# Kernel optimization log

Measured on AMD Instinct MI355X. Metric: run time of the kernel, lower is better.

## Reference

```python
import jax, jax.numpy as jnp
import numpy as np


def _ste_round(x):
    # straight-through rounding (Brevitas-style QAT)
    return x + jax.lax.stop_gradient(jnp.round(x) - x)


def _q_act_signed(x, s):
    # 4-bit signed activation fake-quant: int range [-8, 7]
    return jnp.clip(_ste_round(x / s), -8, 7) * s


def _q_relu(x, s):
    # QuantReLU: relu then 4-bit unsigned fake-quant, int range [0, 15]
    return jnp.clip(_ste_round(jax.nn.relu(x) / s), 0, 15) * s


def _q_weight(w):
    # 4-bit narrow-range per-tensor weight quant: scale = max|w|/7, range [-7, 7]
    s = jnp.max(jnp.abs(w)) / 7.0
    return jnp.clip(_ste_round(w / s), -7, 7) * s, s


def _q_bias(b, s):
    # Int32Bias: bias quantized at scale = act_scale * weight_scale (int32 range, no clamp)
    return _ste_round(b / s) * s


def _conv(x, w):
    return jax.lax.conv_general_dilated(
        x, w, (1, 1), 'VALID', dimension_numbers=('NCHW', 'OIHW', 'NCHW'))


def _maxpool_ceil(x, k=3, st=2):
    # MaxPool2d(3, 2, ceil_mode=True): pad right/bottom with -inf as needed
    def pad(n):
        out = -(-(n - k) // st) + 1
        return max(0, (out - 1) * st + k - n)
    ph, pw = pad(x.shape[2]), pad(x.shape[3])
    return jax.lax.reduce_window(
        x, -jnp.inf, jax.lax.max, (1, 1, k, k), (1, 1, st, st),
        [(0, 0), (0, 0), (0, ph), (0, pw)])


def reference(x, w1, b1, w2, b2, w3, b3, fw1, fb1, bw, bb, cw, cb,
              s_inp, s1, s2, s3, s4, s_bbox, s_conf):
    a = s_inp[0]
    x = _q_act_signed(x, a)                               # quant_inp
    # conv1 + relu1 + pool1
    wq, ws = _q_weight(w1)
    x = _conv(x, wq) + _q_bias(b1, a * ws)[None, :, None, None]
    a = s1[0]
    x = _maxpool_ceil(_q_relu(x, a))                      # [B,28,11,11]
    # conv2 + relu2 + pool2
    wq, ws = _q_weight(w2)
    x = _conv(x, wq) + _q_bias(b2, a * ws)[None, :, None, None]
    a = s2[0]
    x = _maxpool_ceil(_q_relu(x, a))                      # [B,48,4,4]
    # conv3 + relu3
    wq, ws = _q_weight(w3)
    x = _conv(x, wq) + _q_bias(b3, a * ws)[None, :, None, None]
    a = s3[0]
    x = _q_relu(x, a)                                     # [B,64,3,3]
    # QuantFlatten: transpose(3,2) then flatten -> [B, 576]
    x = jnp.transpose(x, (0, 1, 3, 2)).reshape(x.shape[0], -1)
    # fc1 + relu4
    wq, ws = _q_weight(fw1)
    x = x @ wq.T + _q_bias(fb1, a * ws)
    a = s4[0]
    x = _q_relu(x, a)                                     # [B,128]
    # heads
    wq, ws = _q_weight(bw)
    bbox = x @ wq.T + _q_bias(bb, a * ws)                 # [B,4]
    wq, ws = _q_weight(cw)
    conf = x @ wq.T + _q_bias(cb, a * ws)                 # [B,2]
    bbox = _q_act_signed(bbox, s_bbox[0])
    conf = _q_act_signed(conf, s_conf[0])
    return bbox, conf


def setup_inputs() -> dict:
    key = jax.random.key(0)
    ks = jax.random.split(key, 14)
    B = 4096
    f32 = jnp.float32
    return {
        'x': jax.random.normal(ks[0], (B, 3, 24, 24), f32),
        'w1': jax.random.normal(ks[1], (28, 3, 3, 3), f32) * 0.1,
        'b1': jax.random.normal(ks[2], (28,), f32) * 0.1,
        'w2': jax.random.normal(ks[3], (48, 28, 3, 3), f32) * 0.1,
        'b2': jax.random.normal(ks[4], (48,), f32) * 0.1,
        'w3': jax.random.normal(ks[5], (64, 48, 2, 2), f32) * 0.1,
        'b3': jax.random.normal(ks[6], (64,), f32) * 0.1,
        'fw1': jax.random.normal(ks[7], (128, 576), f32) * 0.05,
        'fb1': jax.random.normal(ks[8], (128,), f32) * 0.1,
        'bw': jax.random.normal(ks[9], (4, 128), f32) * 0.1,
        'bb': jax.random.normal(ks[10], (4,), f32) * 0.1,
        'cw': jax.random.normal(ks[11], (2, 128), f32) * 0.1,
        'cb': jax.random.normal(ks[12], (2,), f32) * 0.1,
        's_inp': jnp.ones((1,), f32),
        's1': jnp.ones((1,), f32),
        's2': jnp.ones((1,), f32),
        's3': jnp.ones((1,), f32),
        's4': jnp.ones((1,), f32),
        's_bbox': jnp.ones((1,), f32),
        's_conf': jnp.ones((1,), f32),
    }
```

## Files before the change

### kernel.cpp

```cpp
#include <hip/hip_runtime.h>
#include <hip/hip_bf16.h>
#include <math.h>

typedef __attribute__((ext_vector_type(8))) short bf16x8v;
typedef __attribute__((ext_vector_type(4))) float f32x4v;

__device__ __forceinline__ float loadT(const void* p, size_t i, int isbf) {
    if (isbf) return __bfloat162float(((const __hip_bfloat16*)p)[i]);
    return ((const float*)p)[i];
}
__device__ __forceinline__ float quantw(float v, float s) {
    return fminf(fmaxf(rintf(v / s), -7.f), 7.f) * s;
}
__device__ __forceinline__ float quantwc(float v, float s) {
    return fminf(fmaxf(rintf(v / s), -7.f), 7.f);
}
__device__ __forceinline__ float qbias(float v, float den) {
    return rintf(v / den) * den;
}
__device__ __forceinline__ float qrelu(float v, float s) {
    return fminf(fmaxf(rintf(fmaxf(v, 0.f) / s), 0.f), 15.f) * s;
}
__device__ __forceinline__ float qcode(float Cint, float bcode, float p, float snext) {
    float v = (Cint + bcode) * p;
    return fminf(fmaxf(rintf(fmaxf(v, 0.f) / snext), 0.f), 15.f);
}
__device__ __forceinline__ float bfbits(unsigned u) {
    return __uint_as_float(u << 16);
}

__global__ void k_beacon(float* out, float code) {
    if (threadIdx.x == 0 && blockIdx.x == 0) out[0] = code;
}

static constexpr int W1C  = 16;
static constexpr int B1C  = 772;
static constexpr int B2C  = 800;
static constexpr int B3C  = 848;
static constexpr int FB1C = 912;
static constexpr int BBC  = 1040;
static constexpr int CBC  = 1044;
static constexpr int FW1B = 1048;
static constexpr int W2B  = 37912;
static constexpr int W3B  = 44056;
static constexpr int BWC  = 50200;
static constexpr int CWC  = 50712;
static constexpr int PMAXF = 51000;

__device__ __constant__ int d_CHK[6]  = { 1, 4, 4, 24, 1, 1 };
__device__ __constant__ int d_POFF[7] = { 0, 1, 5, 9, 33, 34, 35 };

__global__ __launch_bounds__(256) void k_scale(
    const void* w1, const void* w2, const void* w3, const void* fw1,
    const void* bw, const void* cw,
    const void* s0p, const void* s1p, const void* s2p, const void* s3p,
    const void* s4p, const void* s5p, const void* s6p,
    float* __restrict__ ws)
{
    __shared__ float red[256];
    __shared__ float shisbf;
    const int tid = threadIdx.x, blk = blockIdx.x;
    if (tid < 64) {
        const unsigned short* hb = (const unsigned short*)w1;
        const float a = fabsf(bfbits((unsigned)hb[2 * tid]));
        const unsigned long long bz = __ballot(a == 0.f);
        const unsigned long long bs = __ballot(a > 1e-8f && a < 1e4f);
        if (tid == 0) {
            const int zeros = __popcll(bz), sane = __popcll(bs);
            shisbf = (zeros < 40 && sane >= 40) ? 1.f : 0.f;
        }
    }
    __syncthreads();
    const int isbf = shisbf > 0.5f;
    if (blk == 0) {
        if (tid == 7) ws[15] = shisbf;
        if (tid < 7) {
            const void* sp[7] = { s0p, s1p, s2p, s3p, s4p, s5p, s6p };
            const void* p = sp[tid];
            float v = *(const float*)p;
            float a = fabsf(v);
            if (!(a > 1e-6f && a < 1e6f)) {
                double d = *(const double*)p;
                double ad = fabs(d);
                if (ad > 1e-6 && ad < 1e6) v = (float)d;
                else v = bfbits((unsigned)(*(const unsigned short*)p));
            }
            ws[tid] = v;
        }
    }
    int j = 0;
    while (j < 5 && blk >= d_POFF[j + 1]) ++j;
    const int c = blk - d_POFF[j];
    const void* wp[6] = { w1, w2, w3, fw1, bw, cw };
    const int   wn[6] = { 756, 12096, 12288, 73728, 512, 256 };
    const int nw = wn[j];
    const int len = (nw + d_CHK[j] - 1) / d_CHK[j];
    const int i0 = c * len, i1 = min(i0 + len, nw);
    float m = 0.f;
    for (int i = i0 + tid; i < i1; i += 256)
        m = fmaxf(m, fabsf(loadT(wp[j], i, isbf)));
    red[tid] = m; __syncthreads();
    for (int o = 128; o > 0; o >>= 1) {
        if (tid < o) red[tid] = fmaxf(red[tid], red[tid + o]);
        __syncthreads();
    }
    if (tid == 0) ws[PMAXF + blk] = red[0];
}

__global__ __launch_bounds__(256) void k_quant(
    const void* w1, const void* b1, const void* w2, const void* b2,
    const void* w3, const void* b3, const void* fw1, const void* fb1,
    const void* bw, const void* bb, const void* cw, const void* cb,
    float* __restrict__ ws)
{
    const int tid = threadIdx.x, blk = blockIdx.x;
    const int isbf = ws[15] > 0.5f;
    auto getscale = [&](int j) {
        float m = 0.f;
        for (int t = d_POFF[j]; t < d_POFF[j + 1]; ++t)
            m = fmaxf(m, ws[PMAXF + t]);
        return m / 7.0f;
    };

    if (blk < 24) {
        const float s = getscale(3);
        const int i0 = blk * 3072, i1 = min(i0 + 3072, 73728);
        __hip_bfloat16* dst = (__hip_bfloat16*)(ws + FW1B);
        for (int i = i0 + tid; i < i1; i += 256) {
            const float q = quantwc(loadT(fw1, i, isbf), s);
            const int o = i / 576, f = i % 576;
            const int c = f / 9, fw_ = (f % 9) / 3, fh = f % 3;
            dst[(c * 9 + fh * 3 + fw_) * 128 + o] = __float2bfloat16(q);
        }
    } else if (blk < 28) {
        const float s = getscale(1);
        const int c = blk - 24;
        const int i0 = c * 3024, i1 = min(i0 + 3024, 12096);
        __hip_bfloat16* dst = (__hip_bfloat16*)(ws + W2B);
        for (int i = i0 + tid; i < i1; i += 256) {
            const float q = quantwc(loadT(w2, i, isbf), s);
            const int n = i / 252, k = i % 252;
            dst[n * 256 + k] = __float2bfloat16(q);
        }
        if (c == 0) {
            for (int i = tid; i < 192; i += 256) {
                const int n = i / 4, k = 252 + (i % 4);
                dst[n * 256 + k] = __float2bfloat16(0.f);
            }
        }
    } else if (blk < 32) {
        const float s = getscale(2);
        const int c = blk - 28;
        const int i0 = c * 3072, i1 = min(i0 + 3072, 12288);
        __hip_bfloat16* dst = (__hip_bfloat16*)(ws + W3B);
        for (int i = i0 + tid; i < i1; i += 256)
            dst[i] = __float2bfloat16(quantwc(loadT(w3, i, isbf), s));
    } else if (blk == 32) {
        const float s = getscale(0);
        for (int i = tid; i < 756; i += 256)
            ws[W1C + i] = quantwc(loadT(w1, i, isbf), s);
    } else {
        const float s0 = getscale(0), s1 = getscale(1), s2 = getscale(2);
        const float s3 = getscale(3), s4 = getscale(4), s5 = getscale(5);
        const float sa0 = ws[0], sa1 = ws[1], sa2 = ws[2], sa3 = ws[3], sa4 = ws[4];
        for (int i = tid; i < 512; i += 256) ws[BWC + i] = quantwc(loadT(bw, i, isbf), s4);
        for (int i = tid; i < 256; i += 256) ws[CWC + i] = quantwc(loadT(cw, i, isbf), s5);
        if (tid < 28)  ws[B1C + tid]  = rintf(loadT(b1, tid, isbf)  / (sa0 * s0));
        if (tid < 48)  ws[B2C + tid]  = rintf(loadT(b2, tid, isbf)  / (sa1 * s1));
        if (tid < 64)  ws[B3C + tid]  = rintf(loadT(b3, tid, isbf)  / (sa2 * s2));
        if (tid < 128) ws[FB1C + tid] = rintf(loadT(fb1, tid, isbf) / (sa3 * s3));
        if (tid < 4)   ws[BBC + tid]  = rintf(loadT(bb, tid, isbf)  / (sa4 * s4));
        if (tid < 2)   ws[CBC + tid]  = rintf(loadT(cb, tid, isbf)  / (sa4 * s5));
        if (tid == 0) {
            ws[8]  = sa0 * s0;
            ws[9]  = sa1 * s1;
            ws[10] = sa2 * s2;
            ws[11] = sa3 * s3;
            ws[12] = sa4 * s4;
            ws[13] = sa4 * s5;
        }
    }
}

__global__ __launch_bounds__(256, 4) void k_net(
    const void* __restrict__ x, const float* __restrict__ wsr,
    float* __restrict__ outp)
{
    __shared__ __align__(16) float U[9952];
    const int tid = threadIdx.x, b = blockIdx.x;
    const float sa0 = wsr[0], sa1 = wsr[1], sa2 = wsr[2], sa3 = wsr[3];
    const float sa4 = wsr[4], sab = wsr[5], sac = wsr[6];
    const float p1 = wsr[8], p2 = wsr[9], p3 = wsr[10], p4 = wsr[11];
    const float pB = wsr[12], pC = wsr[13];
    const int isbf = wsr[15] > 0.5f;
    constexpr int ACT2F = 0, ACT3F = 768, ACT1F = 1344;
    constexpr int XQF = 3040, W1F = 4840, B1F = 5596;
    constexpr int AF = 3040, BFP = 4960, C2IF = 5920, B2CF = 9889;
    constexpr int W3F = 3040, B3CF = 9184;
    constexpr int PF = 3040, A4F = 3296, PARTF = 3424;

    for (int i = tid; i < 1728; i += 256) {
        const float v = loadT(x, (size_t)b * 1728 + i, isbf);
        const int ci = i / 576, r = (i % 576) / 24, c = i % 24;
        U[XQF + ci * 600 + r * 25 + c] = fminf(fmaxf(rintf(v / sa0), -8.f), 7.f);
    }
    for (int i = tid; i < 756; i += 256) U[W1F + i] = wsr[W1C + i];
    if (tid < 28) U[B1F + tid] = wsr[B1C + tid];
    __syncthreads();

    {
        __hip_bfloat16* act1w = (__hip_bfloat16*)(U + ACT1F);
        for (int item = tid; item < 308; item += 256) {
            const int o = item / 11, ph = item % 11;
            const int r0 = 2 * ph;
            const bool row2ok = (r0 + 2) < 22;
            float wk[27];
            #pragma unroll
            for (int i = 0; i < 27; ++i) wk[i] = U[W1F + o * 27 + i];
            const float bc = U[B1F + o];
            float w5[45];
            #pragma unroll
            for (int ci = 0; ci < 3; ++ci)
                #pragma unroll
                for (int ir = 0; ir < 5; ++ir)
                    #pragma unroll
                    for (int j = 0; j < 2; ++j)
                        w5[ci * 15 + ir * 3 + j] =
                            (r0 + ir < 24) ? U[XQF + ci * 600 + (r0 + ir) * 25 + j] : 0.f;
            float accP = -1e30f, accC = -1e30f;
            for (int c = 0; c < 22; ++c) {
                #pragma unroll
                for (int ci = 0; ci < 3; ++ci)
                    #pragma unroll
                    for (int ir = 0; ir < 5; ++ir)
                        w5[ci * 15 + ir * 3 + 2] =
                            (r0 + ir < 24) ? U[XQF + ci * 600 + (r0 + ir) * 25 + (c + 2)] : 0.f;
                float a0 = 0.f, a1 = 0.f, a2 = 0.f;
                #pragma unroll
                for (int ci = 0; ci < 3; ++ci)
                    #pragma unroll
                    for (int kr = 0; kr < 3; ++kr)
                        #pragma unroll
                        for (int kc = 0; kc < 3; ++kc) {
                            const float w = wk[ci * 9 + kr * 3 + kc];
                            a0 = fmaf(w5[ci * 15 + (kr + 0) * 3 + kc], w, a0);
                            a1 = fmaf(w5[ci * 15 + (kr + 1) * 3 + kc], w, a1);
                            a2 = fmaf(w5[ci * 15 + (kr + 2) * 3 + kc], w, a2);
                        }
                float cm = fmaxf(a0, a1);
                cm = row2ok ? fmaxf(cm, a2) : cm;
                if ((c & 1) == 0) {
                    if (c >= 2)
                        act1w[o * 121 + ph * 11 + (c / 2 - 1)] =
                            __float2bfloat16(qcode(fmaxf(accP, cm), bc, p1, sa1));
                    accC = cm;
                } else {
                    accC = fmaxf(accC, cm);
                    accP = accC;
                }
                #pragma unroll
                for (int ci = 0; ci < 3; ++ci)
                    #pragma unroll
                    for (int ir = 0; ir < 5; ++ir) {
                        w5[ci * 15 + ir * 3 + 0] = w5[ci * 15 + ir * 3 + 1];
                        w5[ci * 15 + ir * 3 + 1] = w5[ci * 15 + ir * 3 + 2];
                    }
            }
            act1w[o * 121 + ph * 11 + 10] =
                __float2bfloat16(qcode(accP, bc, p1, sa1));
        }
    }
    __syncthreads();

    {
        const unsigned short* act1u = (const unsigned short*)(U + ACT1F);
        unsigned short* Au = (unsigned short*)(U + AF);
        unsigned short* Bu = (unsigned short*)(U + BFP);
        const unsigned short* w2u = (const unsigned short*)(wsr + W2B);
        if (tid < 48) U[B2CF + tid] = wsr[B2C + tid];
        const int kloc = tid & 31, g = tid >> 5;
        const int wv = tid >> 6, lane = tid & 63;
        f32x4v acc[5];
        #pragma unroll
        for (int j = 0; j < 5; ++j) { acc[j][0]=0.f; acc[j][1]=0.f; acc[j][2]=0.f; acc[j][3]=0.f; }
        for (int kk = 0; kk < 8; ++kk) {
            const int k = kk * 32 + kloc;
            const bool kok = (k < 252);
            const int ci = kok ? k / 9 : 0;
            const int kr = kok ? (k % 9) / 3 : 0, kc = kok ? k % 3 : 0;
            #pragma unroll
            for (int e = 0; e < 12; ++e) {
                const int s = g + 8 * e;
                unsigned short v = 0;
                if (kok && s < 81) {
                    const int r = s / 9, c = s % 9;
                    v = act1u[ci * 121 + (r + kr) * 11 + (c + kc)];
                }
                Au[s * 40 + kloc] = v;
            }
            #pragma unroll
            for (int e = 0; e < 6; ++e) {
                const int n = g + 8 * e;
                Bu[n * 40 + kloc] = w2u[n * 256 + k];
            }
            __syncthreads();
            #pragma unroll
            for (int j = 0; j < 5; ++j) {
                const int t = wv + 4 * j;
                if (t < 18) {
                    const int tm = t / 3, tn = t % 3;
                    bf16x8v af = *(const bf16x8v*)(Au + (tm * 16 + (lane & 15)) * 40 + (lane >> 4) * 8);
                    bf16x8v bfv = *(const bf16x8v*)(Bu + (tn * 16 + (lane & 15)) * 40 + (lane >> 4) * 8);
                    acc[j] = __builtin_amdgcn_mfma_f32_16x16x32_bf16(af, bfv, acc[j], 0, 0, 0);
                }
            }
            __syncthreads();
        }
        #pragma unroll
        for (int j = 0; j < 5; ++j) {
            const int t = wv + 4 * j;
            if (t < 18) {
                const int tm = t / 3, tn = t % 3;
                const int col = tn * 16 + (lane & 15);
                #pragma unroll
                for (int r = 0; r < 4; ++r) {
                    const int row = tm * 16 + (lane >> 4) * 4 + r;
                    if (row < 81) U[C2IF + row * 49 + col] = acc[j][r];
                }
            }
        }
        __syncthreads();
        for (int id = tid; id < 768; id += 256) {
            const int ch = id >> 4, pp = id & 15, ph = pp >> 2, pw = pp & 3;
            float mx = -1e30f;
            #pragma unroll
            for (int r = 0; r < 3; ++r)
                #pragma unroll
                for (int c = 0; c < 3; ++c)
                    mx = fmaxf(mx, U[C2IF + ((2 * ph + r) * 9 + (2 * pw + c)) * 49 + ch]);
            U[ACT2F + ch * 16 + pp] = qcode(mx, U[B2CF + ch], p2, sa2);
        }
    }
    __syncthreads();

    for (int i = tid; i < 6144; i += 256) U[W3F + i] = wsr[W3B + i];
    if (tid < 64) U[B3CF + tid] = wsr[B3C + tid];
    __syncthreads();
    if (tid < 192) {
        const int o = tid / 3, hq = tid % 3;
        const unsigned* w3u = (const unsigned*)(U + W3F);
        float a0 = 0.f, a1 = 0.f, a2 = 0.f;
        for (int ci = 0; ci < 48; ++ci) {
            const unsigned pa = w3u[o * 96 + ci * 2];
            const unsigned pb = w3u[o * 96 + ci * 2 + 1];
            const float w00 = bfbits(pa & 0xffffu), w01 = bfbits(pa >> 16);
            const float w10 = bfbits(pb & 0xffffu), w11 = bfbits(pb >> 16);
            const int xb = ACT2F + ci * 16;
            float r0[4], r1[4];
            #pragma unroll
            for (int c = 0; c < 4; ++c) {
                r0[c] = U[xb + hq * 4 + c];
                r1[c] = U[xb + (hq + 1) * 4 + c];
            }
            a0 = fmaf(r0[0], w00, a0); a0 = fmaf(r0[1], w01, a0);
            a0 = fmaf(r1[0], w10, a0); a0 = fmaf(r1[1], w11, a0);
            a1 = fmaf(r0[1], w00, a1); a1 = fmaf(r0[2], w01, a1);
            a1 = fmaf(r1[1], w10, a1); a1 = fmaf(r1[2], w11, a1);
            a2 = fmaf(r0[2], w00, a2); a2 = fmaf(r0[3], w01, a2);
            a2 = fmaf(r1[2], w10, a2); a2 = fmaf(r1[3], w11, a2);
        }
        const float bc = U[B3CF + o];
        U[ACT3F + o * 9 + hq * 3 + 0] = qcode(a0, bc, p3, sa3);
        U[ACT3F + o * 9 + hq * 3 + 1] = qcode(a1, bc, p3, sa3);
        U[ACT3F + o * 9 + hq * 3 + 2] = qcode(a2, bc, p3, sa3);
    }
    __syncthreads();

    {
        const int o = tid & 127, half = tid >> 7;
        const __hip_bfloat16* fwb = (const __hip_bfloat16*)(wsr + FW1B);
        float acc = 0.f;
        const int k0 = half * 288;
        for (int k = k0; k < k0 + 288; ++k)
            acc = fmaf(U[ACT3F + k], __bfloat162float(fwb[k * 128 + o]), acc);
        U[PF + tid] = acc;
    }
    __syncthreads();
    if (tid < 128) {
        const float C = U[PF + tid] + U[PF + 128 + tid];
        U[A4F + tid] = qcode(C, wsr[FB1C + tid], p4, sa4);
    }
    __syncthreads();

    if (tid < 96) {
        const int d = tid >> 4, gq = tid & 15;
        const float* hw = (d < 4) ? (wsr + BWC + d * 128) : (wsr + CWC + (d - 4) * 128);
        float p = 0.f;
        #pragma unroll
        for (int k = 0; k < 8; ++k)
            p = fmaf(U[A4F + gq * 8 + k], hw[gq * 8 + k], p);
        U[PARTF + d * 16 + gq] = p;
    }
    __syncthreads();
    if (tid < 6) {
        float C = (tid < 4) ? wsr[BBC + tid] : wsr[CBC + (tid - 4)];
        for (int g = 0; g < 16; ++g) C += U[PARTF + tid * 16 + g];
        if (tid < 4) {
            const float val = C * pB;
            outp[(size_t)b * 4 + tid] = fminf(fmaxf(rintf(val / sab), -8.f), 7.f) * sab;
        } else {
            const float val = C * pC;
            outp[16384 + (size_t)b * 2 + (tid - 4)] =
                fminf(fmaxf(rintf(val / sac), -8.f), 7.f) * sac;
        }
    }
}

__global__ __launch_bounds__(256) void k_net_fb(
    const void* __restrict__ x,
    const void* __restrict__ w1,  const void* __restrict__ b1,
    const void* __restrict__ w2,  const void* __restrict__ b2,
    const void* __restrict__ w3,  const void* __restrict__ b3,
    const void* __restrict__ fw1, const void* __restrict__ fb1,
    const void* __restrict__ bw,  const void* __restrict__ bb,
    const void* __restrict__ cw,  const void* __restrict__ cb,
    const void* __restrict__ s0p, const void* __restrict__ s1p,
    const void* __restrict__ s2p, const void* __restrict__ s3p,
    const void* __restrict__ s4p, const void* __restrict__ s5p,
    const void* __restrict__ s6p,
    float* __restrict__ outp)
{
    __shared__ float U[16000];
    __shared__ float swsh[8];
    __shared__ float sash[8];
    const int tid = threadIdx.x;
    const int b   = blockIdx.x;
    constexpr int RED = 0, XQ = 0, W1Q = 1728, B1Q = 2484, C1 = 2512;
    constexpr int ACT1 = 9288, WB = 0, C2 = 12676, ACT2 = 14620, ACT3 = 15388;
    constexpr int A4 = 0, PART = 128;

    if (tid == 0) {
        const unsigned short* hb = (const unsigned short*)w1;
        int zeros = 0, sane = 0;
        for (int i = 0; i < 64; ++i) {
            unsigned short u = hb[2 * i];
            float v = __uint_as_float(((unsigned int)u) << 16);
            float a = fabsf(v);
            if (a == 0.f) zeros++;
            else if (a > 1e-8f && a < 1e4f) sane++;
        }
        swsh[7] = (zeros < 40 && sane >= 40) ? 1.f : 0.f;
        const void* sp[7] = { s0p, s1p, s2p, s3p, s4p, s5p, s6p };
        for (int j = 0; j < 7; ++j) {
            float v = *(const float*)sp[j];
            float a = fabsf(v);
            if (!(a > 1e-6f && a < 1e6f)) {
                double d = *(const double*)sp[j];
                double ad = fabs(d);
                if (ad > 1e-6 && ad < 1e6) v = (float)d;
                else {
                    unsigned short u = *(const unsigned short*)sp[j];
                    v = __uint_as_float(((unsigned int)u) << 16);
                }
            }
            sash[j] = v;
        }
    }
    __syncthreads();
    const int isbf = swsh[7] > 0.5f;
    {
        const void* wp[6] = { w1, w2, w3, fw1, bw, cw };
        const int   wn[6] = { 756, 12096, 12288, 73728, 512, 256 };
        for (int j = 0; j < 6; ++j) {
            float m = 0.f;
            for (int i = tid; i < wn[j]; i += 256)
                m = fmaxf(m, fabsf(loadT(wp[j], i, isbf)));
            U[RED + tid] = m; __syncthreads();
            for (int o = 128; o > 0; o >>= 1) {
                if (tid < o) U[RED + tid] = fmaxf(U[RED + tid], U[RED + tid + o]);
                __syncthreads();
            }
            if (tid == 0) swsh[j] = U[RED] / 7.0f;
            __syncthreads();
        }
    }
    const float sa0 = sash[0], sa1 = sash[1], sa2 = sash[2], sa3 = sash[3];
    const float sa4 = sash[4], sab = sash[5], sac = sash[6];
    const float sw1s = swsh[0], sw2s = swsh[1], sw3s = swsh[2];
    const float sw4s = swsh[3], swbs = swsh[4], swcs = swsh[5];

    for (int i = tid; i < 1728; i += 256) {
        float v = loadT(x, (size_t)b * 1728 + i, isbf);
        U[XQ + i] = fminf(fmaxf(rintf(v / sa0), -8.f), 7.f) * sa0;
    }
    for (int i = tid; i < 756; i += 256) U[W1Q + i] = quantw(loadT(w1, i, isbf), sw1s);
    {
        const float den = sa0 * sw1s;
        for (int i = tid; i < 28; i += 256) U[B1Q + i] = qbias(loadT(b1, i, isbf), den);
    }
    __syncthreads();

    for (int g = 0; g < 2; ++g) {
        const int obase = g * 14;
        for (int idx = tid; idx < 308; idx += 256) {
            const int ol = idx / 22, r = idx % 22, o = obase + ol;
            for (int c = 0; c < 22; ++c) {
                float acc = 0.f;
                #pragma unroll
                for (int ci = 0; ci < 3; ++ci)
                    #pragma unroll
                    for (int kr = 0; kr < 3; ++kr)
                        #pragma unroll
                        for (int kc = 0; kc < 3; ++kc)
                            acc = fmaf(U[XQ + ci * 576 + (r + kr) * 24 + (c + kc)],
                                       U[W1Q + o * 27 + ci * 9 + kr * 3 + kc], acc);
                U[C1 + ol * 484 + r * 22 + c] = acc + U[B1Q + o];
            }
        }
        __syncthreads();
        for (int i = tid; i < 1694; i += 256) {
            const int ol = i / 121, rem = i % 121, ph = rem / 11, pw = rem % 11;
            const int r0 = 2 * ph, c0 = 2 * pw;
            const int r1 = min(r0 + 3, 22), c1 = min(c0 + 3, 22);
            float mx = -1e30f;
            for (int r = r0; r < r1; ++r)
                for (int c = c0; c < c1; ++c)
                    mx = fmaxf(mx, U[C1 + ol * 484 + r * 22 + c]);
            U[ACT1 + (obase + ol) * 121 + rem] = qrelu(mx, sa1);
        }
        __syncthreads();
    }

    for (int h = 0; h < 2; ++h) {
        const int obase = h * 24;
        for (int i = tid; i < 6048; i += 256)
            U[WB + i] = quantw(loadT(w2, (size_t)h * 6048 + i, isbf), sw2s);
        {
            const float den = sa1 * sw2s;
            for (int i = tid; i < 24; i += 256)
                U[WB + 6048 + i] = qbias(loadT(b2, obase + i, isbf), den);
        }
        __syncthreads();
        for (int idx = tid; idx < 216; idx += 256) {
            const int ol = idx / 9, r = idx % 9;
            for (int c = 0; c < 9; ++c) {
                float acc = 0.f;
                for (int ci = 0; ci < 28; ++ci)
                    #pragma unroll
                    for (int kr = 0; kr < 3; ++kr)
                        #pragma unroll
                        for (int kc = 0; kc < 3; ++kc)
                            acc = fmaf(U[ACT1 + ci * 121 + (r + kr) * 11 + (c + kc)],
                                       U[WB + ol * 252 + ci * 9 + kr * 3 + kc], acc);
                U[C2 + ol * 81 + r * 9 + c] = acc + U[WB + 6048 + ol];
            }
        }
        __syncthreads();
        for (int i = tid; i < 384; i += 256) {
            const int ol = i / 16, ph = (i % 16) / 4, pw = i % 4;
            float mx = -1e30f;
            #pragma unroll
            for (int r = 0; r < 3; ++r)
                #pragma unroll
                for (int c = 0; c < 3; ++c)
                    mx = fmaxf(mx, U[C2 + ol * 81 + (2 * ph + r) * 9 + (2 * pw + c)]);
            U[ACT2 + (obase + ol) * 16 + (i % 16)] = qrelu(mx, sa2);
        }
        __syncthreads();
    }

    for (int h = 0; h < 2; ++h) {
        const int obase = h * 32;
        for (int i = tid; i < 6144; i += 256)
            U[WB + i] = quantw(loadT(w3, (size_t)h * 6144 + i, isbf), sw3s);
        {
            const float den = sa2 * sw3s;
            for (int i = tid; i < 32; i += 256)
                U[WB + 6144 + i] = qbias(loadT(b3, obase + i, isbf), den);
        }
        __syncthreads();
        for (int idx = tid; idx < 288; idx += 256) {
            const int ol = idx / 9, hh = (idx % 9) / 3, ww = idx % 3;
            float acc = 0.f;
            for (int ci = 0; ci < 48; ++ci) {
                const int xb2 = ACT2 + ci * 16;
                const int wb2 = WB + ol * 192 + ci * 4;
                acc = fmaf(U[xb2 + hh * 4 + ww],           U[wb2 + 0], acc);
                acc = fmaf(U[xb2 + hh * 4 + ww + 1],       U[wb2 + 1], acc);
                acc = fmaf(U[xb2 + (hh + 1) * 4 + ww],     U[wb2 + 2], acc);
                acc = fmaf(U[xb2 + (hh + 1) * 4 + ww + 1], U[wb2 + 3], acc);
            }
            acc += U[WB + 6144 + ol];
            U[ACT3 + (obase + ol) * 9 + hh * 3 + ww] = qrelu(acc, sa3);
        }
        __syncthreads();
    }

    {
        const int wave = tid >> 6, lane = tid & 63;
        const float den = sa3 * sw4s;
        for (int oo = 0; oo < 32; ++oo) {
            const int o = wave * 32 + oo;
            float acc = 0.f;
            #pragma unroll
            for (int j = 0; j < 9; ++j) {
                const int f = lane + 64 * j;
                const int c = f / 9, fw = (f % 9) / 3, fh = f % 3;
                const float av = U[ACT3 + c * 9 + fh * 3 + fw];
                const float wv = quantw(loadT(fw1, (size_t)o * 576 + f, isbf), sw4s);
                acc = fmaf(av, wv, acc);
            }
            #pragma unroll
            for (int off = 32; off > 0; off >>= 1)
                acc += __shfl_down(acc, off);
            if (lane == 0) {
                acc += qbias(loadT(fb1, o, isbf), den);
                U[A4 + o] = qrelu(acc, sa4);
            }
        }
    }
    __syncthreads();

    if (tid < 96) {
        const int d = tid >> 4, g = tid & 15;
        const void* hw = (d < 4) ? bw : cw;
        const int row = (d < 4) ? d : d - 4;
        const float swh = (d < 4) ? swbs : swcs;
        float p = 0.f;
        #pragma unroll
        for (int k = 0; k < 8; ++k) {
            const int kk = g * 8 + k;
            p = fmaf(U[A4 + kk], quantw(loadT(hw, row * 128 + kk, isbf), swh), p);
        }
        U[PART + d * 16 + g] = p;
    }
    __syncthreads();
    if (tid < 6) {
        const int d = tid;
        float acc;
        if (d < 4) acc = qbias(loadT(bb, d, isbf), sa4 * swbs);
        else       acc = qbias(loadT(cb, d - 4, isbf), sa4 * swcs);
        for (int g = 0; g < 16; ++g) acc += U[PART + d * 16 + g];
        if (d < 4) outp[(size_t)b * 4 + d] = fminf(fmaxf(rintf(acc / sab), -8.f), 7.f) * sab;
        else outp[16384 + (size_t)b * 2 + (d - 4)] = fminf(fmaxf(rintf(acc / sac), -8.f), 7.f) * sac;
    }
}

extern "C" void kernel_launch(void* const* d_in, const int* in_sizes, int n_in,
                              void* d_out, int out_size, void* d_ws, size_t ws_size,
                              hipStream_t stream)
{
    float* out = (float*)d_out;
    const int expect[20] = { 7077888, 756, 28, 12096, 48, 12288, 64, 73728, 128,
                             512, 4, 256, 2, 1, 1, 1, 1, 1, 1, 1 };
    if (n_in < 20) { k_beacon<<<1, 64, 0, stream>>>(out, 9000.f); return; }
    for (int i = 0; i < 20; ++i)
        if (in_sizes[i] != expect[i]) {
            k_beacon<<<1, 64, 0, stream>>>(out, 2000.f + 10.f * i);
            return;
        }

    if (ws_size >= (size_t)100000 * sizeof(float)) {
        float* ws = (float*)d_ws;
        k_scale<<<35, 256, 0, stream>>>(
            d_in[1], d_in[3], d_in[5], d_in[7], d_in[9], d_in[11],
            d_in[13], d_in[14], d_in[15], d_in[16], d_in[17], d_in[18], d_in[19],
            ws);
        k_quant<<<34, 256, 0, stream>>>(
            d_in[1], d_in[2], d_in[3], d_in[4], d_in[5], d_in[6],
            d_in[7], d_in[8], d_in[9], d_in[10], d_in[11], d_in[12],
            ws);
        k_net<<<4096, 256, 0, stream>>>(d_in[0], ws, out);
    } else {
        k_net_fb<<<4096, 256, 0, stream>>>(
            d_in[0], d_in[1], d_in[2], d_in[3], d_in[4], d_in[5], d_in[6],
            d_in[7], d_in[8], d_in[9], d_in[10], d_in[11], d_in[12],
            d_in[13], d_in[14], d_in[15], d_in[16], d_in[17], d_in[18], d_in[19],
            out);
    }
}
```

Measured before the change: 224.1 us.

## Run conv1 as bf16 MFMA im2col GEMM with separate maxpool pass

Conv1 moves from a per-thread scalar FMA sliding window to an im2col GEMM on 16x16x32 bf16 MFMA. The quantized input and the weights, padded to 32 per output channel, are stored as bf16. Conv outputs go to an fp16 shared buffer in two row halves, and a second pass does the 3x3/2 max-pool, bias and quant. The conv2 im2col gather also precomputes per-row and per-k offsets to drop divisions in the inner loop. Intermediates are small integers, so bf16/fp16 should stay exact, but the change adds extra syncs and a shared-memory round trip.

```diff
diff --git a/kernel.cpp b/kernel.cpp
--- a/kernel.cpp
+++ b/kernel.cpp
@@ -4,6 +4,7 @@
 
 typedef __attribute__((ext_vector_type(8))) short bf16x8v;
 typedef __attribute__((ext_vector_type(4))) float f32x4v;
+typedef __attribute__((ext_vector_type(2))) _Float16 f16x2;
 
 __device__ __forceinline__ float loadT(const void* p, size_t i, int isbf) {
     if (isbf) return __bfloat162float(((const __hip_bfloat16*)p)[i]);
@@ -46,6 +47,7 @@
 static constexpr int BWC  = 50200;
 static constexpr int CWC  = 50712;
 static constexpr int PMAXF = 51000;
+static constexpr int W1BF  = 51100;
 
 __device__ __constant__ int d_CHK[6]  = { 1, 4, 4, 24, 1, 1 };
 __device__ __constant__ int d_POFF[7] = { 0, 1, 5, 9, 33, 34, 35 };
@@ -157,8 +159,13 @@
             dst[i] = __float2bfloat16(quantwc(loadT(w3, i, isbf), s));
     } else if (blk == 32) {
         const float s = getscale(0);
-        for (int i = tid; i < 756; i += 256)
-            ws[W1C + i] = quantwc(loadT(w1, i, isbf), s);
+        __hip_bfloat16* dst = (__hip_bfloat16*)(ws + W1BF);
+        for (int i = tid; i < 1024; i += 256) {
+            const int o = i >> 5, k = i & 31;
+            float q = 0.f;
+            if (o < 28 && k < 27) q = quantwc(loadT(w1, (size_t)o * 27 + k, isbf), s);
+            dst[i] = __float2bfloat16(q);
+        }
     } else {
         const float s0 = getscale(0), s1 = getscale(1), s2 = getscale(2);
         const float s3 = getscale(3), s4 = getscale(4), s5 = getscale(5);
@@ -194,83 +201,91 @@
     const float pB = wsr[12], pC = wsr[13];
     const int isbf = wsr[15] > 0.5f;
     constexpr int ACT2F = 0, ACT3F = 768, ACT1F = 1344;
-    constexpr int XQF = 3040, W1F = 4840, B1F = 5596;
+    constexpr int XQF = 3040;
+    constexpr int C1F = 4224;
+    constexpr int B1CF = 8576;
     constexpr int AF = 3040, BFP = 4960, C2IF = 5920, B2CF = 9889;
     constexpr int W3F = 3040, B3CF = 9184;
     constexpr int PF = 3040, A4F = 3296, PARTF = 3424;
 
-    for (int i = tid; i < 1728; i += 256) {
-        const float v = loadT(x, (size_t)b * 1728 + i, isbf);
-        const int ci = i / 576, r = (i % 576) / 24, c = i % 24;
-        U[XQF + ci * 600 + r * 25 + c] = fminf(fmaxf(rintf(v / sa0), -8.f), 7.f);
-    }
-    for (int i = tid; i < 756; i += 256) U[W1F + i] = wsr[W1C + i];
-    if (tid < 28) U[B1F + tid] = wsr[B1C + tid];
-    __syncthreads();
-
     {
+        __hip_bfloat16* xqw = (__hip_bfloat16*)(U + XQF);
+        for (int i = tid; i < 1728; i += 256) {
+            const float v = loadT(x, (size_t)b * 1728 + i, isbf);
+            const int ci = i / 576, r = (i % 576) / 24, c = i % 24;
+            xqw[ci * 600 + r * 25 + c] =
+                __float2bfloat16(fminf(fmaxf(rintf(v / sa0), -8.f), 7.f));
+        }
+        for (int i = tid; i < 284; i += 256) U[XQF + 900 + i] = 0.f;
+        if (tid < 28) U[B1CF + tid] = wsr[B1C + tid];
+    }
+    __syncthreads();
+
+    {
+        const unsigned short* xqb = (const unsigned short*)(U + XQF);
         __hip_bfloat16* act1w = (__hip_bfloat16*)(U + ACT1F);
-        for (int item = tid; item < 308; item += 256) {
-            const int o = item / 11, ph = item % 11;
-            const int r0 = 2 * ph;
-            const bool row2ok = (r0 + 2) < 22;
-            float wk[27];
-            #pragma unroll
-            for (int i = 0; i < 27; ++i) wk[i] = U[W1F + o * 27 + i];
-            const float bc = U[B1F + o];
-            float w5[45];
-            #pragma unroll
-            for (int ci = 0; ci < 3; ++ci)
+        _Float16* C1h = (_Float16*)(U + C1F);
+        const int lane = tid & 63, wv = tid >> 6;
+        const int kg = lane >> 4, col = lane & 15;
+        int offj[8]; unsigned short mskj[8];
+        #pragma unroll
+        for (int j = 0; j < 8; ++j) {
+            const int k = kg * 8 + j;
+            const int ci = k / 9, rem = k - 9 * ci, kr = rem / 3, kc = rem - 3 * kr;
+            offj[j] = ci * 600 + kr * 25 + kc;
+            mskj[j] = (k < 27) ? (unsigned short)0xffffu : (unsigned short)0;
+        }
+        bf16x8v b1f[2];
+        {
+            const unsigned short* w1b = (const unsigned short*)(wsr + W1BF);
+            #pragma unroll
+            for (int tn = 0; tn < 2; ++tn)
+                b1f[tn] = *(const bf16x8v*)(w1b + (tn * 16 + col) * 32 + kg * 8);
+        }
+        #pragma unroll
+        for (int h = 0; h < 2; ++h) {
+            const int R0 = h ? 10 : 0;
+            const int nt = h ? 17 : 16;
+            for (int t = wv; t < nt; t += 4) {
+                const int sA = t * 16 + col;
+                const int r = sA / 22, c = sA - 22 * r;
+                const int base = (R0 + r) * 25 + c;
+                bf16x8v af;
                 #pragma unroll
-                for (int ir = 0; ir < 5; ++ir)
-                    #pragma unroll
-                    for (int j = 0; j < 2; ++j)
-                        w5[ci * 15 + ir * 3 + j] =
-                            (r0 + ir < 24) ? U[XQF + ci * 600 + (r0 + ir) * 25 + j] : 0.f;
-            float accP = -1e30f, accC = -1e30f;
-            for (int c = 0; c < 22; ++c) {
+                for (int j = 0; j < 8; ++j)
+                    af[j] = (short)(xqb[base + offj[j]] & mskj[j]);
                 #pragma unroll
-                for (int ci = 0; ci < 3; ++ci)
-                    #pragma unroll
-                    for (int ir = 0; ir < 5; ++ir)
-                        w5[ci * 15 + ir * 3 + 2] =
-                            (r0 + ir < 24) ? U[XQF + ci * 600 + (r0 + ir) * 25 + (c + 2)] : 0.f;
-                float a0 = 0.f, a1 = 0.f, a2 = 0.f;
-                #pragma unroll
-                for (int ci = 0; ci < 3; ++ci)
-                    #pragma unroll
-                    for (int kr = 0; kr < 3; ++kr)
-                        #pragma unroll
-                        for (int kc = 0; kc < 3; ++kc) {
-                            const float w = wk[ci * 9 + kr * 3 + kc];
-                            a0 = fmaf(w5[ci * 15 + (kr + 0) * 3 + kc], w, a0);
-                            a1 = fmaf(w5[ci * 15 + (kr + 1) * 3 + kc], w, a1);
-                            a2 = fmaf(w5[ci * 15 + (kr + 2) * 3 + kc], w, a2);
-                        }
-                float cm = fmaxf(a0, a1);
-                cm = row2ok ? fmaxf(cm, a2) : cm;
-                if ((c & 1) == 0) {
-                    if (c >= 2)
-                        act1w[o * 121 + ph * 11 + (c / 2 - 1)] =
-                            __float2bfloat16(qcode(fmaxf(accP, cm), bc, p1, sa1));
-                    accC = cm;
-                } else {
-                    accC = fmaxf(accC, cm);
-                    accP = accC;
+                for (int tn = 0; tn < 2; ++tn) {
+                    f32x4v acc = { 0.f, 0.f, 0.f, 0.f };
+                    acc = __builtin_amdgcn_mfma_f32_16x16x32_bf16(af, b1f[tn], acc, 0, 0, 0);
+                    const int ch = tn * 16 + col;
+                    if (ch < 28) {
+                        const int sc = t * 16 + (kg << 2);
+                        f16x2 lo = { (_Float16)acc[0], (_Float16)acc[1] };
+                        f16x2 hi = { (_Float16)acc[2], (_Float16)acc[3] };
+                        *(f16x2*)(C1h + ch * 272 + sc)     = lo;
+                        *(f16x2*)(C1h + ch * 272 + sc + 2) = hi;
+                    }
                 }
-                #pragma unroll
-                for (int ci = 0; ci < 3; ++ci)
-                    #pragma unroll
-                    for (int ir = 0; ir < 5; ++ir) {
-                        w5[ci * 15 + ir * 3 + 0] = w5[ci * 15 + ir * 3 + 1];
-                        w5[ci * 15 + ir * 3 + 1] = w5[ci * 15 + ir * 3 + 2];
-                    }
-            }
-            act1w[o * 121 + ph * 11 + 10] =
-                __float2bfloat16(qcode(accP, bc, p1, sa1));
-        }
-    }
-    __syncthreads();
+            }
+            __syncthreads();
+            const int P0 = h ? 5 : 0, NP = h ? 6 : 5;
+            const int nout = 28 * NP * 11;
+            for (int id = tid; id < nout; id += 256) {
+                const int o = id / (NP * 11), rem2 = id % (NP * 11);
+                const int ph = P0 + rem2 / 11, pw = rem2 % 11;
+                const int rg0 = 2 * ph, c0 = 2 * pw;
+                const int rg1 = min(rg0 + 3, 22), c1 = min(c0 + 3, 22);
+                float mx = -1e30f;
+                for (int rg = rg0; rg < rg1; ++rg)
+                    for (int c = c0; c < c1; ++c)
+                        mx = fmaxf(mx, (float)C1h[o * 272 + (rg - R0) * 22 + c]);
+                act1w[o * 121 + ph * 11 + pw] =
+                    __float2bfloat16(qcode(mx, U[B1CF + o], p1, sa1));
+            }
+            __syncthreads();
+        }
+    }
 
     {
         const unsigned short* act1u = (const unsigned short*)(U + ACT1F);
@@ -280,23 +295,30 @@
         if (tid < 48) U[B2CF + tid] = wsr[B2C + tid];
         const int kloc = tid & 31, g = tid >> 5;
         const int wv = tid >> 6, lane = tid & 63;
+        int sb[12]; bool svld[12];
+        #pragma unroll
+        for (int e = 0; e < 12; ++e) {
+            const int s = g + 8 * e;
+            const int r = s / 9;
+            sb[e] = s + 2 * r;
+            svld[e] = (s < 81);
+        }
         f32x4v acc[5];
         #pragma unroll
         for (int j = 0; j < 5; ++j) { acc[j][0]=0.f; acc[j][1]=0.f; acc[j][2]=0.f; acc[j][3]=0.f; }
         for (int kk = 0; kk < 8; ++kk) {
             const int k = kk * 32 + kloc;
             const bool kok = (k < 252);
-            const int ci = kok ? k / 9 : 0;
-            const int kr = kok ? (k % 9) / 3 : 0, kc = kok ? k % 3 : 0;
+            int koff = 0;
+            if (kok) {
+                const int ci = k / 9, rem = k - 9 * ci, kr = rem / 3, kc = rem - 3 * kr;
+                koff = ci * 121 + kr * 11 + kc;
+            }
             #pragma unroll
             for (int e = 0; e < 12; ++e) {
                 const int s = g + 8 * e;
-                unsigned short v = 0;
-                if (kok && s < 81) {
-                    const int r = s / 9, c = s % 9;
-                    v = act1u[ci * 121 + (r + kr) * 11 + (c + kc)];
-                }
-                Au[s * 40 + kloc] = v;
+                Au[s * 40 + kloc] =
+                    (kok && svld[e]) ? act1u[koff + sb[e]] : (unsigned short)0;
             }
             #pragma unroll
             for (int e = 0; e < 6; ++e) {
```

New measurement: 241.3 us. 1.08x slower.
